# Kernel tuning notes

Measured on AMD Instinct MI355X. Metric: run time of the kernel, lower is better.

## Reference

```python
import jax, jax.numpy as jnp
import numpy as np

L, N, E = 2048, 2, 512
H = 8
HD = E // H
FF = 2048
NLAYERS = 2
EPS = 1e-5


def setup_inputs() -> dict:
    key = jax.random.key(0)
    ks = jax.random.split(key, 8)
    s = 0.02
    return {
        "src": jax.random.normal(ks[0], (L, N, E), jnp.float32),
        # packed qkv projection, torch Linear convention: y = x @ W.T + b
        "in_proj_w": jax.random.normal(ks[1], (NLAYERS, 3 * E, E), jnp.float32) * s,
        "in_proj_b": jnp.zeros((NLAYERS, 3 * E), jnp.float32),
        "out_proj_w": jax.random.normal(ks[2], (NLAYERS, E, E), jnp.float32) * s,
        "out_proj_b": jnp.zeros((NLAYERS, E), jnp.float32),
        "lin1_w": jax.random.normal(ks[3], (NLAYERS, FF, E), jnp.float32) * s,
        "lin1_b": jnp.zeros((NLAYERS, FF), jnp.float32),
        "lin2_w": jax.random.normal(ks[4], (NLAYERS, E, FF), jnp.float32) * s,
        "lin2_b": jnp.zeros((NLAYERS, E), jnp.float32),
        "ln1_g": jnp.ones((NLAYERS, E), jnp.float32),
        "ln1_b": jnp.zeros((NLAYERS, E), jnp.float32),
        "ln2_g": jnp.ones((NLAYERS, E), jnp.float32),
        "ln2_b": jnp.zeros((NLAYERS, E), jnp.float32),
    }


def _layer_norm(x, g, b):
    mu = jnp.mean(x, axis=-1, keepdims=True)
    var = jnp.mean(jnp.square(x - mu), axis=-1, keepdims=True)
    return (x - mu) * jax.lax.rsqrt(var + EPS) * g + b


def _mha(x, w_qkv, b_qkv, w_o, b_o):
    # x: [L, N, E] (seq-first, as in torch multi_head_attention_forward)
    qkv = jnp.einsum('lne,fe->lnf', x, w_qkv) + b_qkv  # [L, N, 3E]
    q, k, v = jnp.split(qkv, 3, axis=-1)
    q = q.reshape(L, N, H, HD) * (1.0 / np.sqrt(HD))  # torch scales q pre-bmm
    k = k.reshape(L, N, H, HD)
    v = v.reshape(L, N, H, HD)
    scores = jnp.einsum('lnhd,snhd->nhls', q, k)  # [N, H, L, S] -- O(L*S) matrix
    attn = jax.nn.softmax(scores, axis=-1)
    o = jnp.einsum('nhls,snhd->lnhd', attn, v).reshape(L, N, E)
    return jnp.einsum('lne,fe->lnf', o, w_o) + b_o


def reference(src, in_proj_w, in_proj_b, out_proj_w, out_proj_b,
              lin1_w, lin1_b, lin2_w, lin2_b, ln1_g, ln1_b, ln2_g, ln2_b):
    x = src
    for i in range(NLAYERS):  # fixed small layer count
        a = _mha(x, in_proj_w[i], in_proj_b[i], out_proj_w[i], out_proj_b[i])
        x = _layer_norm(x + a, ln1_g[i], ln1_b[i])  # post-norm (torch default)
        h = jax.nn.relu(jnp.einsum('lne,fe->lnf', x, lin1_w[i]) + lin1_b[i])
        f = jnp.einsum('lnf,ef->lne', h, lin2_w[i]) + lin2_b[i]
        x = _layer_norm(x + f, ln2_g[i], ln2_b[i])
    return x
```

## Files before the change

### kernel.cpp

```cpp
#include <hip/hip_runtime.h>
#include <hip/hip_bf16.h>

using bf16 = __hip_bfloat16;
typedef __bf16 bf16x8 __attribute__((ext_vector_type(8)));
typedef float f32x4 __attribute__((ext_vector_type(4)));

#define MFMA(a, b, c) __builtin_amdgcn_mfma_f32_16x16x32_bf16(a, b, c, 0, 0, 0)

constexpr int L = 2048, N = 2, E = 512, H = 8, HD = 64, FF = 2048;
constexpr int T = L * N;

__global__ void detect_dtype(const unsigned int* __restrict__ g,
                             int* __restrict__ flag) {
  if (threadIdx.x == 0 && blockIdx.x == 0)
    *flag = (g[0] != 0x3F800000u) ? 1 : 0;
}

__global__ __launch_bounds__(256) void cvt_to_bf16(
    const void* __restrict__ in, bf16* __restrict__ out, int n,
    const int* __restrict__ flag) {
  int i = (blockIdx.x * 256 + threadIdx.x) * 8;
  if (i >= n) return;
  if (*flag) {
    *(uint4*)&out[i] = *(const uint4*)&((const bf16*)in)[i];
  } else {
    float4 a = *(const float4*)&((const float*)in)[i];
    float4 b = *(const float4*)&((const float*)in)[i + 4];
    bf16 o8[8] = {__float2bfloat16(a.x), __float2bfloat16(a.y),
                  __float2bfloat16(a.z), __float2bfloat16(a.w),
                  __float2bfloat16(b.x), __float2bfloat16(b.y),
                  __float2bfloat16(b.z), __float2bfloat16(b.w)};
    *(uint4*)&out[i] = *(const uint4*)o8;
  }
}

__global__ __launch_bounds__(256) void cvt_to_f32(
    const void* __restrict__ in, float* __restrict__ out, int n,
    const int* __restrict__ flag) {
  int i = blockIdx.x * 256 + threadIdx.x;
  if (i >= n) return;
  out[i] = (*flag) ? __bfloat162float(((const bf16*)in)[i])
                   : ((const float*)in)[i];
}

__device__ __forceinline__ void gload16(const bf16* g, bf16* l) {
  __builtin_amdgcn_global_load_lds(
      (const __attribute__((address_space(1))) unsigned int*)g,
      (__attribute__((address_space(3))) unsigned int*)l, 16, 0, 0);
}

template <bool RELU, int FN>
__global__ __launch_bounds__(256) void gemm_bt(
    const bf16* __restrict__ A, const bf16* __restrict__ W,
    const float* __restrict__ bias, bf16* __restrict__ C,
    int M, int F, int K) {
  constexpr int BN = FN * 32;
  __shared__ __align__(16) bf16 As[2][64 * 32];
  __shared__ __align__(16) bf16 Bs[2][BN * 32];
  const int bm = blockIdx.x, bn = blockIdx.y;
  const int tid = threadIdx.x;
  const int w = tid >> 6, lane = tid & 63;
  const int wr = w >> 1, wc = w & 1;
  const int lhi = lane >> 4, llo = lane & 15;
  f32x4 acc[2][FN] = {};

  const bf16* ap = &A[(size_t)(bm * 64 + (tid >> 2)) * K + (tid & 3) * 8];
  const bf16* wp[FN / 2];
#pragma unroll
  for (int s = 0; s < FN / 2; ++s) {
    int c = tid + s * 256;
    wp[s] = &W[(size_t)(bn * BN + (c >> 2)) * K + (c & 3) * 8];
  }

  auto stage = [&](int buf, int k0) {
    gload16(ap + k0, &As[buf][tid * 8]);
#pragma unroll
    for (int s = 0; s < FN / 2; ++s)
      gload16(wp[s] + k0, &Bs[buf][(tid + s * 256) * 8]);
  };

  stage(0, 0);
  int cur = 0;
  for (int k0 = 0; k0 < K; k0 += 32) {
    __syncthreads();
    if (k0 + 32 < K) stage(cur ^ 1, k0 + 32);
    bf16x8 af[2], bfr[FN];
#pragma unroll
    for (int mi = 0; mi < 2; ++mi)
      af[mi] =
          *(const bf16x8*)&As[cur][(wr * 32 + mi * 16 + llo) * 32 + lhi * 8];
#pragma unroll
    for (int ni = 0; ni < FN; ++ni)
      bfr[ni] = *(const bf16x8*)&Bs[cur]
          [(wc * FN * 16 + ni * 16 + llo) * 32 + lhi * 8];
#pragma unroll
    for (int mi = 0; mi < 2; ++mi)
#pragma unroll
      for (int ni = 0; ni < FN; ++ni)
        acc[mi][ni] = MFMA(af[mi], bfr[ni], acc[mi][ni]);
    cur ^= 1;
  }
#pragma unroll
  for (int mi = 0; mi < 2; ++mi) {
#pragma unroll
    for (int ni = 0; ni < FN; ++ni) {
      int col = bn * BN + wc * FN * 16 + ni * 16 + llo;
      float bv = bias[col];
#pragma unroll
      for (int r = 0; r < 4; ++r) {
        int row = bm * 64 + wr * 32 + mi * 16 + lhi * 4 + r;
        float v = acc[mi][ni][r] + bv;
        if (RELU) v = fmaxf(v, 0.f);
        C[(size_t)row * F + col] = __float2bfloat16(v);
      }
    }
  }
}

constexpr int QB = 64, KB = 64, LDA = 72;

__global__ __launch_bounds__(256) void attn_split(
    const bf16* __restrict__ qkv, float* __restrict__ opart,
    float* __restrict__ lpart) {
  __shared__ __align__(16) bf16 Qs[QB * LDA];
  __shared__ __align__(16) bf16 Ks[KB * LDA];
  __shared__ __align__(16) bf16 VT[HD * 80];
  __shared__ __align__(16) bf16 Ps[QB * LDA];
  const int blk = blockIdx.x;
  const int qb = blk & 31;
  const int nh = (blk >> 5) & 15;
  const int split = blk >> 9;
  const int n = nh >> 3, h = nh & 7;
  const int tid = threadIdx.x;
  const int w = tid >> 6, lane = tid & 63;
  const int lhi = lane >> 4, llo = lane & 15;
  const int kb0 = split * 16, kb1 = kb0 + 16;

#pragma unroll
  for (int s = 0; s < 2; ++s) {
    int c = tid + s * 256;
    int i = c >> 3, dc = c & 7;
    size_t t = (size_t)((qb * QB + i) * N + n);
    *(uint4*)&Qs[i * LDA + dc * 8] =
        *(const uint4*)&qkv[t * 1536 + h * 64 + dc * 8];
  }
  __syncthreads();
  bf16x8 aq[2];
  aq[0] = *(const bf16x8*)&Qs[(w * 16 + llo) * LDA + 0 + lhi * 8];
  aq[1] = *(const bf16x8*)&Qs[(w * 16 + llo) * LDA + 32 + lhi * 8];

  uint4 kreg[2], vreg[2];
  auto load_regs = [&](int kb) {
#pragma unroll
    for (int s = 0; s < 2; ++s) {
      int c = tid + s * 256;
      int j = c >> 3, dc = c & 7;
      size_t t = (size_t)((kb * KB + j) * N + n);
      kreg[s] = *(const uint4*)&qkv[t * 1536 + 512 + h * 64 + dc * 8];
      vreg[s] = *(const uint4*)&qkv[t * 1536 + 1024 + h * 64 + dc * 8];
    }
  };
  load_regs(kb0);

  float psum[4] = {0.f, 0.f, 0.f, 0.f};
  f32x4 o[4] = {};

  for (int kb = kb0; kb < kb1; ++kb) {
    __syncthreads();
#pragma unroll
    for (int s = 0; s < 2; ++s) {
      int c = tid + s * 256;
      int j = c >> 3, dc = c & 7;
      *(uint4*)&Ks[j * LDA + dc * 8] = kreg[s];
      const bf16* ve = (const bf16*)&vreg[s];
      char* vb = (char*)VT + (((j >> 3) ^ dc) << 4) + ((j & 7) << 1);
#pragma unroll
      for (int e = 0; e < 8; ++e)
        *(bf16*)(vb + (dc * 8 + e) * 160) = ve[e];
    }
    if (kb + 1 < kb1) load_regs(kb + 1);
    __syncthreads();

    f32x4 sfr[4] = {};
    __builtin_amdgcn_s_setprio(1);
#pragma unroll
    for (int cb = 0; cb < 4; ++cb) {
#pragma unroll
      for (int ks = 0; ks < 2; ++ks) {
        bf16x8 b =
            *(const bf16x8*)&Ks[(cb * 16 + llo) * LDA + ks * 32 + lhi * 8];
        sfr[cb] = MFMA(aq[ks], b, sfr[cb]);
      }
    }
    __builtin_amdgcn_s_setprio(0);

#pragma unroll
    for (int cb = 0; cb < 4; ++cb) {
#pragma unroll
      for (int r = 0; r < 4; ++r) {
        float p = __expf(sfr[cb][r] * 0.125f);
        psum[r] += p;
        Ps[(w * 16 + lhi * 4 + r) * LDA + cb * 16 + llo] = __float2bfloat16(p);
      }
    }
    asm volatile("" ::: "memory");
    __builtin_amdgcn_s_setprio(1);
#pragma unroll
    for (int cb = 0; cb < 4; ++cb) {
      const int crow = cb * 16 + llo;
#pragma unroll
      for (int ks = 0; ks < 2; ++ks) {
        bf16x8 a =
            *(const bf16x8*)&Ps[(w * 16 + llo) * LDA + ks * 32 + lhi * 8];
        bf16x8 b = *(const bf16x8*)((const char*)VT + crow * 160 +
                                    (((ks * 4 + lhi) ^ (crow >> 3)) << 4));
        o[cb] = MFMA(a, b, o[cb]);
      }
    }
    __builtin_amdgcn_s_setprio(0);
  }

#pragma unroll
  for (int r = 0; r < 4; ++r) {
    float v = psum[r];
#pragma unroll
    for (int d = 1; d < 16; d <<= 1) v += __shfl_xor(v, d);
    psum[r] = v;
  }
#pragma unroll
  for (int cb = 0; cb < 4; ++cb) {
#pragma unroll
    for (int r = 0; r < 4; ++r) {
      int i = w * 16 + lhi * 4 + r;
      int d = cb * 16 + llo;
      size_t t = (size_t)((qb * QB + i) * N + n);
      opart[((size_t)split * T + t) * E + h * 64 + d] = o[cb][r];
    }
  }
  if (llo == 0) {
#pragma unroll
    for (int r = 0; r < 4; ++r) {
      int i = w * 16 + lhi * 4 + r;
      size_t t = (size_t)((qb * QB + i) * N + n);
      lpart[(size_t)(split * T + t) * H + h] = psum[r];
    }
  }
}

__global__ __launch_bounds__(256) void attn_merge(
    const float* __restrict__ opart, const float* __restrict__ lpart,
    bf16* __restrict__ atn) {
  int i = (blockIdx.x * 256 + threadIdx.x) * 4;
  if (i >= T * E) return;
  int t = i >> 9;
  int h = (i >> 6) & 7;
  float4 o0 = *(const float4*)&opart[i];
  float4 o1 = *(const float4*)&opart[(size_t)T * E + i];
  float rl = 1.f / (lpart[(size_t)t * H + h] + lpart[(size_t)(T + t) * H + h]);
  bf16 r4[4] = {__float2bfloat16((o0.x + o1.x) * rl),
                __float2bfloat16((o0.y + o1.y) * rl),
                __float2bfloat16((o0.z + o1.z) * rl),
                __float2bfloat16((o0.w + o1.w) * rl)};
  *(uint2*)&atn[i] = *(const uint2*)r4;
}

template <typename OutT>
__global__ __launch_bounds__(256) void add_ln(
    const bf16* __restrict__ res, const bf16* __restrict__ y,
    const float* __restrict__ g, const float* __restrict__ b,
    OutT* __restrict__ out) {
  const int t = blockIdx.x;
  const int tid = threadIdx.x;
  const int w = tid >> 6, lane = tid & 63;
  const int e = tid * 2;
  const size_t base = (size_t)t * E;
  float v0 = __bfloat162float(res[base + e]) + __bfloat162float(y[base + e]);
  float v1 = __bfloat162float(res[base + e + 1]) + __bfloat162float(y[base + e + 1]);
  float s = v0 + v1, q = v0 * v0 + v1 * v1;
#pragma unroll
  for (int d = 1; d < 64; d <<= 1) {
    s += __shfl_xor(s, d);
    q += __shfl_xor(q, d);
  }
  __shared__ float rs[4], rq[4];
  if (lane == 0) { rs[w] = s; rq[w] = q; }
  __syncthreads();
  float S = rs[0] + rs[1] + rs[2] + rs[3];
  float Qq = rq[0] + rq[1] + rq[2] + rq[3];
  float mu = S * (1.f / E);
  float var = Qq * (1.f / E) - mu * mu;
  float rstd = rsqrtf(var + 1e-5f);
  float o0 = (v0 - mu) * rstd * g[e] + b[e];
  float o1 = (v1 - mu) * rstd * g[e + 1] + b[e + 1];
  if constexpr (__is_same(OutT, float)) {
    out[base + e] = o0;
    out[base + e + 1] = o1;
  } else {
    out[base + e] = __float2bfloat16(o0);
    out[base + e + 1] = __float2bfloat16(o1);
  }
}

extern "C" void kernel_launch(void* const* d_in, const int* in_sizes, int n_in,
                              void* d_out, int out_size, void* d_ws,
                              size_t ws_size, hipStream_t stream) {
  int* flag = (int*)d_ws;
  float* pbuf = (float*)((char*)d_ws + 16);
  float* in_b = pbuf;
  float* ob   = in_b + 3072;
  float* l1b  = ob + 1024;
  float* l2b  = l1b + 4096;
  float* ln1g = l2b + 1024;
  float* ln1b = ln1g + 1024;
  float* ln2g = ln1b + 1024;
  float* ln2b = ln2g + 1024;
  bf16* big  = (bf16*)(ln2b + 1024);
  bf16* srcb = big;
  bf16* in_w = srcb + (size_t)T * E;
  bf16* ow   = in_w + (size_t)2 * 1536 * E;
  bf16* l1w  = ow + (size_t)2 * E * E;
  bf16* l2w  = l1w + (size_t)2 * FF * E;
  bf16* qkv  = l2w + (size_t)2 * E * FF;
  bf16* atn  = qkv + (size_t)T * 1536;
  bf16* ybuf = atn + (size_t)T * E;
  bf16* x1   = ybuf + (size_t)T * E;
  bf16* x2   = x1 + (size_t)T * E;
  bf16* hbuf = x2 + (size_t)T * E;
  float* opart = (float*)hbuf;
  float* lpart = (float*)ybuf;

  detect_dtype<<<1, 64, 0, stream>>>((const unsigned int*)d_in[9], flag);
  auto cvtb = [&](const void* in, bf16* out, int n) {
    cvt_to_bf16<<<dim3(n / 2048), 256, 0, stream>>>(in, out, n, flag);
  };
  auto cvtf = [&](const void* in, float* out, int n) {
    cvt_to_f32<<<dim3(n / 256), 256, 0, stream>>>(in, out, n, flag);
  };
  cvtb(d_in[0], srcb, T * E);
  cvtb(d_in[1], in_w, 2 * 1536 * E);
  cvtb(d_in[3], ow, 2 * E * E);
  cvtb(d_in[5], l1w, 2 * FF * E);
  cvtb(d_in[7], l2w, 2 * E * FF);
  cvtf(d_in[2], in_b, 3072);
  cvtf(d_in[4], ob, 1024);
  cvtf(d_in[6], l1b, 4096);
  cvtf(d_in[8], l2b, 1024);
  cvtf(d_in[9], ln1g, 1024);
  cvtf(d_in[10], ln1b, 1024);
  cvtf(d_in[11], ln2g, 1024);
  cvtf(d_in[12], ln2b, 1024);

  const bf16* x = srcb;
  for (int i = 0; i < 2; ++i) {
    gemm_bt<false, 4><<<dim3(T / 64, 1536 / 128), 256, 0, stream>>>(
        x, in_w + (size_t)i * 1536 * E, in_b + i * 1536, qkv, T, 1536, E);
    attn_split<<<dim3(1024), 256, 0, stream>>>(qkv, opart, lpart);
    attn_merge<<<dim3(T * E / 1024), 256, 0, stream>>>(opart, lpart, atn);
    gemm_bt<false, 2><<<dim3(T / 64, E / 64), 256, 0, stream>>>(
        atn, ow + (size_t)i * E * E, ob + i * E, ybuf, T, E, E);
    add_ln<bf16><<<dim3(T), 256, 0, stream>>>(
        x, ybuf, ln1g + i * E, ln1b + i * E, x1);
    gemm_bt<true, 4><<<dim3(T / 64, FF / 128), 256, 0, stream>>>(
        x1, l1w + (size_t)i * FF * E, l1b + i * FF, hbuf, T, FF, E);
    gemm_bt<false, 2><<<dim3(T / 64, E / 64), 256, 0, stream>>>(
        hbuf, l2w + (size_t)i * E * FF, l2b + i * E, ybuf, T, E, FF);
    if (i == 1) {
      add_ln<float><<<dim3(T), 256, 0, stream>>>(
          x1, ybuf, ln2g + i * E, ln2b + i * E, (float*)d_out);
    } else {
      add_ln<bf16><<<dim3(T), 256, 0, stream>>>(
          x1, ybuf, ln2g + i * E, ln2b + i * E, x2);
    }
    x = x2;
  }
}
```

Baseline: 348.5 us.

## Pre-transpose K/V into swizzled tiles and use 128x128 GEMM tiles

Adds a prep_kv kernel that writes K and transposed V into contiguous, XOR-swizzled 64x64 tiles in global memory. The attention kernel can then stream them straight into double-buffered LDS with async global-to-LDS loads, with no per-iteration register staging, scalar V transpose or extra barrier. Separately, the QKV and FFN1 GEMMs move to a 128x128 block tile with a 4x4 MFMA accumulator per wave to raise data reuse. The cost is an extra kernel launch, an extra global round trip for K and V, more LDS, and fewer blocks for the big GEMMs.

```diff
diff --git a/kernel.cpp b/kernel.cpp
--- a/kernel.cpp
+++ b/kernel.cpp
@@ -49,34 +49,33 @@
       (__attribute__((address_space(3))) unsigned int*)l, 16, 0, 0);
 }
 
-template <bool RELU, int FN>
-__global__ __launch_bounds__(256) void gemm_bt(
+template <bool RELU>
+__global__ __launch_bounds__(256) void gemm128(
     const bf16* __restrict__ A, const bf16* __restrict__ W,
     const float* __restrict__ bias, bf16* __restrict__ C,
     int M, int F, int K) {
-  constexpr int BN = FN * 32;
-  __shared__ __align__(16) bf16 As[2][64 * 32];
-  __shared__ __align__(16) bf16 Bs[2][BN * 32];
+  __shared__ __align__(16) bf16 As[2][128 * 32];
+  __shared__ __align__(16) bf16 Bs[2][128 * 32];
   const int bm = blockIdx.x, bn = blockIdx.y;
   const int tid = threadIdx.x;
   const int w = tid >> 6, lane = tid & 63;
   const int wr = w >> 1, wc = w & 1;
   const int lhi = lane >> 4, llo = lane & 15;
-  f32x4 acc[2][FN] = {};
-
-  const bf16* ap = &A[(size_t)(bm * 64 + (tid >> 2)) * K + (tid & 3) * 8];
-  const bf16* wp[FN / 2];
-#pragma unroll
-  for (int s = 0; s < FN / 2; ++s) {
+  f32x4 acc[4][4] = {};
+
+  const bf16 *ap[2], *wp[2];
+#pragma unroll
+  for (int s = 0; s < 2; ++s) {
     int c = tid + s * 256;
-    wp[s] = &W[(size_t)(bn * BN + (c >> 2)) * K + (c & 3) * 8];
-  }
-
+    ap[s] = &A[(size_t)(bm * 128 + (c >> 2)) * K + (c & 3) * 8];
+    wp[s] = &W[(size_t)(bn * 128 + (c >> 2)) * K + (c & 3) * 8];
+  }
   auto stage = [&](int buf, int k0) {
-    gload16(ap + k0, &As[buf][tid * 8]);
-#pragma unroll
-    for (int s = 0; s < FN / 2; ++s)
+#pragma unroll
+    for (int s = 0; s < 2; ++s) {
+      gload16(ap[s] + k0, &As[buf][(tid + s * 256) * 8]);
       gload16(wp[s] + k0, &Bs[buf][(tid + s * 256) * 8]);
+    }
   };
 
   stage(0, 0);
@@ -84,27 +83,86 @@
   for (int k0 = 0; k0 < K; k0 += 32) {
     __syncthreads();
     if (k0 + 32 < K) stage(cur ^ 1, k0 + 32);
-    bf16x8 af[2], bfr[FN];
+    bf16x8 af[4], bfr[4];
+#pragma unroll
+    for (int mi = 0; mi < 4; ++mi)
+      af[mi] =
+          *(const bf16x8*)&As[cur][(wr * 64 + mi * 16 + llo) * 32 + lhi * 8];
+#pragma unroll
+    for (int ni = 0; ni < 4; ++ni)
+      bfr[ni] =
+          *(const bf16x8*)&Bs[cur][(wc * 64 + ni * 16 + llo) * 32 + lhi * 8];
+#pragma unroll
+    for (int mi = 0; mi < 4; ++mi)
+#pragma unroll
+      for (int ni = 0; ni < 4; ++ni)
+        acc[mi][ni] = MFMA(af[mi], bfr[ni], acc[mi][ni]);
+    cur ^= 1;
+  }
+#pragma unroll
+  for (int mi = 0; mi < 4; ++mi) {
+#pragma unroll
+    for (int ni = 0; ni < 4; ++ni) {
+      int col = bn * 128 + wc * 64 + ni * 16 + llo;
+      float bv = bias[col];
+#pragma unroll
+      for (int r = 0; r < 4; ++r) {
+        int row = bm * 128 + wr * 64 + mi * 16 + lhi * 4 + r;
+        float v = acc[mi][ni][r] + bv;
+        if (RELU) v = fmaxf(v, 0.f);
+        C[(size_t)row * F + col] = __float2bfloat16(v);
+      }
+    }
+  }
+}
+
+template <bool RELU>
+__global__ __launch_bounds__(256) void gemm64(
+    const bf16* __restrict__ A, const bf16* __restrict__ W,
+    const float* __restrict__ bias, bf16* __restrict__ C,
+    int M, int F, int K) {
+  __shared__ __align__(16) bf16 As[2][64 * 32];
+  __shared__ __align__(16) bf16 Bs[2][64 * 32];
+  const int bm = blockIdx.x, bn = blockIdx.y;
+  const int tid = threadIdx.x;
+  const int w = tid >> 6, lane = tid & 63;
+  const int wr = w >> 1, wc = w & 1;
+  const int lhi = lane >> 4, llo = lane & 15;
+  f32x4 acc[2][2] = {};
+
+  const bf16* ap = &A[(size_t)(bm * 64 + (tid >> 2)) * K + (tid & 3) * 8];
+  const bf16* wp = &W[(size_t)(bn * 64 + (tid >> 2)) * K + (tid & 3) * 8];
+  auto stage = [&](int buf, int k0) {
+    gload16(ap + k0, &As[buf][tid * 8]);
+    gload16(wp + k0, &Bs[buf][tid * 8]);
+  };
+
+  stage(0, 0);
+  int cur = 0;
+  for (int k0 = 0; k0 < K; k0 += 32) {
+    __syncthreads();
+    if (k0 + 32 < K) stage(cur ^ 1, k0 + 32);
+    bf16x8 af[2], bfr[2];
 #pragma unroll
     for (int mi = 0; mi < 2; ++mi)
       af[mi] =
           *(const bf16x8*)&As[cur][(wr * 32 + mi * 16 + llo) * 32 + lhi * 8];
 #pragma unroll
-    for (int ni = 0; ni < FN; ++ni)
-      bfr[ni] = *(const bf16x8*)&Bs[cur]
-          [(wc * FN * 16 + ni * 16 + llo) * 32 + lhi * 8];
+    for (int ni = 0; ni < 2; ++ni)
+      bfr[ni] =
+          *(const bf16x8*)&Bs[cur][(wc * 32 + ni * 16 + llo) * 32 + lhi * 8];
 #pragma unroll
     for (int mi = 0; mi < 2; ++mi)
 #pragma unroll
-      for (int ni = 0; ni < FN; ++ni)
+      for (int ni = 0; ni < 2; ++ni)
         acc[mi][ni] = MFMA(af[mi], bfr[ni], acc[mi][ni]);
     cur ^= 1;
   }
 #pragma unroll
   for (int mi = 0; mi < 2; ++mi) {
 #pragma unroll
-    for (int ni = 0; ni < FN; ++ni) {
-      int col = bn * BN + wc * FN * 16 + ni * 16 + llo;
+    for (int ni = 0; ni < 2; ++ni) {
+      int col = bn * 64 + wc * 32 + ni * 16 + llo;
       float bv = bias[col];
 #pragma unroll
       for (int r = 0; r < 4; ++r) {
@@ -117,15 +175,46 @@
   }
 }
 
-constexpr int QB = 64, KB = 64, LDA = 72;
+__global__ __launch_bounds__(256) void prep_kv(
+    const bf16* __restrict__ qkv, bf16* __restrict__ kt,
+    bf16* __restrict__ vt) {
+  __shared__ __align__(16) bf16 Vl[64 * 72];
+  const int blk = blockIdx.x;
+  const int kb = blk & 31, nh = blk >> 5;
+  const int n = nh >> 3, h = nh & 7;
+  const int tid = threadIdx.x;
+  bf16* ko = kt + ((size_t)nh * 32 + kb) * 4096;
+  bf16* vo = vt + ((size_t)nh * 32 + kb) * 4096;
+#pragma unroll
+  for (int s = 0; s < 2; ++s) {
+    int c = tid + s * 256;
+    int jj = c >> 3, g = c & 7;
+    size_t t = (size_t)((kb * 64 + jj) * N + n);
+    uint4 kk = *(const uint4*)&qkv[t * 1536 + 512 + h * 64 + g * 8];
+    *(uint4*)&ko[jj * 64 + ((g ^ (jj & 7)) * 8)] = kk;
+    uint4 vv = *(const uint4*)&qkv[t * 1536 + 1024 + h * 64 + g * 8];
+    *(uint4*)&Vl[jj * 72 + g * 8] = vv;
+  }
+  __syncthreads();
+#pragma unroll
+  for (int s = 0; s < 2; ++s) {
+    int c = tid + s * 256;
+    int d = c >> 3, gsw = c & 7;
+    int g = gsw ^ (d & 7);
+    bf16 tmp[8];
+#pragma unroll
+    for (int e = 0; e < 8; ++e) tmp[e] = Vl[(g * 8 + e) * 72 + d];
+    *(uint4*)&vo[d * 64 + gsw * 8] = *(const uint4*)tmp;
+  }
+}
 
 __global__ __launch_bounds__(256) void attn_split(
-    const bf16* __restrict__ qkv, float* __restrict__ opart,
+    const bf16* __restrict__ qkv, const bf16* __restrict__ kt,
+    const bf16* __restrict__ vt, float* __restrict__ opart,
     float* __restrict__ lpart) {
-  __shared__ __align__(16) bf16 Qs[QB * LDA];
-  __shared__ __align__(16) bf16 Ks[KB * LDA];
-  __shared__ __align__(16) bf16 VT[HD * 80];
-  __shared__ __align__(16) bf16 Ps[QB * LDA];
+  __shared__ __align__(16) bf16 Kb[2][4096];
+  __shared__ __align__(16) bf16 Vb[2][4096];
+  __shared__ __align__(16) bf16 Ps[64 * 72];
   const int blk = blockIdx.x;
   const int qb = blk & 31;
   const int nh = (blk >> 5) & 15;
@@ -140,55 +229,44 @@
   for (int s = 0; s < 2; ++s) {
     int c = tid + s * 256;
     int i = c >> 3, dc = c & 7;
-    size_t t = (size_t)((qb * QB + i) * N + n);
-    *(uint4*)&Qs[i * LDA + dc * 8] =
+    size_t t = (size_t)((qb * 64 + i) * N + n);
+    *(uint4*)&Ps[i * 72 + dc * 8] =
         *(const uint4*)&qkv[t * 1536 + h * 64 + dc * 8];
   }
   __syncthreads();
   bf16x8 aq[2];
-  aq[0] = *(const bf16x8*)&Qs[(w * 16 + llo) * LDA + 0 + lhi * 8];
-  aq[1] = *(const bf16x8*)&Qs[(w * 16 + llo) * LDA + 32 + lhi * 8];
-
-  uint4 kreg[2], vreg[2];
-  auto load_regs = [&](int kb) {
+  aq[0] = *(const bf16x8*)&Ps[(w * 16 + llo) * 72 + 0 + lhi * 8];
+  aq[1] = *(const bf16x8*)&Ps[(w * 16 + llo) * 72 + 32 + lhi * 8];
+
+  const bf16* ktile = kt + (size_t)nh * 32 * 4096;
+  const bf16* vtile = vt + (size_t)nh * 32 * 4096;
+  auto stage = [&](int buf, int kb) {
 #pragma unroll
     for (int s = 0; s < 2; ++s) {
       int c = tid + s * 256;
-      int j = c >> 3, dc = c & 7;
-      size_t t = (size_t)((kb * KB + j) * N + n);
-      kreg[s] = *(const uint4*)&qkv[t * 1536 + 512 + h * 64 + dc * 8];
-      vreg[s] = *(const uint4*)&qkv[t * 1536 + 1024 + h * 64 + dc * 8];
+      gload16(ktile + (size_t)kb * 4096 + c * 8, &Kb[buf][c * 8]);
+      gload16(vtile + (size_t)kb * 4096 + c * 8, &Vb[buf][c * 8]);
     }
   };
-  load_regs(kb0);
+  stage(0, kb0);
 
   float psum[4] = {0.f, 0.f, 0.f, 0.f};
   f32x4 o[4] = {};
+  int cur = 0;
 
   for (int kb = kb0; kb < kb1; ++kb) {
     __syncthreads();
-#pragma unroll
-    for (int s = 0; s < 2; ++s) {
-      int c = tid + s * 256;
-      int j = c >> 3, dc = c & 7;
-      *(uint4*)&Ks[j * LDA + dc * 8] = kreg[s];
-      const bf16* ve = (const bf16*)&vreg[s];
-      char* vb = (char*)VT + (((j >> 3) ^ dc) << 4) + ((j & 7) << 1);
-#pragma unroll
-      for (int e = 0; e < 8; ++e)
-        *(bf16*)(vb + (dc * 8 + e) * 160) = ve[e];
-    }
-    if (kb + 1 < kb1) load_regs(kb + 1);
-    __syncthreads();
+    if (kb + 1 < kb1) stage(cur ^ 1, kb + 1);
 
     f32x4 sfr[4] = {};
     __builtin_amdgcn_s_setprio(1);
 #pragma unroll
     for (int cb = 0; cb < 4; ++cb) {
+      const int row = cb * 16 + llo;
 #pragma unroll
       for (int ks = 0; ks < 2; ++ks) {
-        bf16x8 b =
-            *(const bf16x8*)&Ks[(cb * 16 + llo) * LDA + ks * 32 + lhi * 8];
+        bf16x8 b = *(const bf16x8*)&Kb[cur]
+            [row * 64 + (((ks * 4 + lhi) ^ (row & 7)) << 3)];
         sfr[cb] = MFMA(aq[ks], b, sfr[cb]);
       }
     }
@@ -200,10 +278,11 @@
       for (int r = 0; r < 4; ++r) {
         float p = __expf(sfr[cb][r] * 0.125f);
         psum[r] += p;
-        Ps[(w * 16 + lhi * 4 + r) * LDA + cb * 16 + llo] = __float2bfloat16(p);
+        Ps[(w * 16 + lhi * 4 + r) * 72 + cb * 16 + llo] = __float2bfloat16(p);
       }
     }
     asm volatile("" ::: "memory");
+
     __builtin_amdgcn_s_setprio(1);
 #pragma unroll
     for (int cb = 0; cb < 4; ++cb) {
@@ -211,13 +290,14 @@
 #pragma unroll
       for (int ks = 0; ks < 2; ++ks) {
         bf16x8 a =
-            *(const bf16x8*)&Ps[(w * 16 + llo) * LDA + ks * 32 + lhi * 8];
-        bf16x8 b = *(const bf16x8*)((const char*)VT + crow * 160 +
-                                    (((ks * 4 + lhi) ^ (crow >> 3)) << 4));
+            *(const bf16x8*)&Ps[(w * 16 + llo) * 72 + ks * 32 + lhi * 8];
+        bf16x8 b = *(const bf16x8*)&Vb[cur]
+            [crow * 64 + (((ks * 4 + lhi) ^ (crow & 7)) << 3)];
         o[cb] = MFMA(a, b, o[cb]);
       }
     }
     __builtin_amdgcn_s_setprio(0);
+    cur ^= 1;
   }
 
 #pragma unroll
@@ -233,7 +313,7 @@
     for (int r = 0; r < 4; ++r) {
       int i = w * 16 + lhi * 4 + r;
       int d = cb * 16 + llo;
-      size_t t = (size_t)((qb * QB + i) * N + n);
+      size_t t = (size_t)((qb * 64 + i) * N + n);
       opart[((size_t)split * T + t) * E + h * 64 + d] = o[cb][r];
     }
   }
@@ -241,7 +321,7 @@
 #pragma unroll
     for (int r = 0; r < 4; ++r) {
       int i = w * 16 + lhi * 4 + r;
-      size_t t = (size_t)((qb * QB + i) * N + n);
+      size_t t = (size_t)((qb * 64 + i) * N + n);
       lpart[(size_t)(split * T + t) * H + h] = psum[r];
     }
   }
@@ -326,6 +406,8 @@
   bf16* x1   = ybuf + (size_t)T * E;
   bf16* x2   = x1 + (size_t)T * E;
   bf16* hbuf = x2 + (size_t)T * E;
+  bf16* ktg  = hbuf + (size_t)T * FF;
+  bf16* vtg  = ktg + (size_t)T * E;
   float* opart = (float*)hbuf;
   float* lpart = (float*)ybuf;
 
@@ -352,17 +434,18 @@
 
   const bf16* x = srcb;
   for (int i = 0; i < 2; ++i) {
-    gemm_bt<false, 4><<<dim3(T / 64, 1536 / 128), 256, 0, stream>>>(
+    gemm128<false><<<dim3(T / 128, 1536 / 128), 256, 0, stream>>>(
         x, in_w + (size_t)i * 1536 * E, in_b + i * 1536, qkv, T, 1536, E);
-    attn_split<<<dim3(1024), 256, 0, stream>>>(qkv, opart, lpart);
+    prep_kv<<<dim3(512), 256, 0, stream>>>(qkv, ktg, vtg);
+    attn_split<<<dim3(1024), 256, 0, stream>>>(qkv, ktg, vtg, opart, lpart);
     attn_merge<<<dim3(T * E / 1024), 256, 0, stream>>>(opart, lpart, atn);
-    gemm_bt<false, 2><<<dim3(T / 64, E / 64), 256, 0, stream>>>(
+    gemm64<false><<<dim3(T / 64, E / 64), 256, 0, stream>>>(
         atn, ow + (size_t)i * E * E, ob + i * E, ybuf, T, E, E);
     add_ln<bf16><<<dim3(T), 256, 0, stream>>>(
         x, ybuf, ln1g + i * E, ln1b + i * E, x1);
-    gemm_bt<true, 4><<<dim3(T / 64, FF / 128), 256, 0, stream>>>(
+    gemm128<true><<<dim3(T / 128, FF / 128), 256, 0, stream>>>(
         x1, l1w + (size_t)i * FF * E, l1b + i * FF, hbuf, T, FF, E);
-    gemm_bt<false, 2><<<dim3(T / 64, E / 64), 256, 0, stream>>>(
+    gemm64<false><<<dim3(T / 64, E / 64), 256, 0, stream>>>(
         hbuf, l2w + (size_t)i * E * FF, l2b + i * E, ybuf, T, E, FF);
     if (i == 1) {
       add_ln<float><<<dim3(T), 256, 0, stream>>>(
```

Result: faster. 326.4 us (-6.3%).
